# Kernel tuning notes

Measured on AMD Instinct MI355X. Metric: run time of the kernel, lower is better.

## Reference

```python
import jax, jax.numpy as jnp
import numpy as np

N_NODES = 100000
N_EDGES = 1000000
D_IN = 64
D_OUT = 64


def setup_inputs() -> dict:
    key = jax.random.key(0)
    k1, k2, k3, k4, k5 = jax.random.split(key, 5)
    x = jax.random.normal(k1, (N_NODES, D_IN), dtype=jnp.float32)
    W = jax.random.normal(k2, (D_OUT, D_IN), dtype=jnp.float32) / np.sqrt(D_IN)
    edge_weights = jax.random.uniform(k3, (N_EDGES,), dtype=jnp.float32)
    source = jax.random.randint(k4, (N_EDGES,), 0, N_NODES, dtype=jnp.int64 if jax.config.read('jax_enable_x64') else jnp.int32)
    target = jax.random.randint(k5, (N_EDGES,), 0, N_NODES, dtype=jnp.int64 if jax.config.read('jax_enable_x64') else jnp.int32)
    return {"x": x, "W": W, "edge_weights": edge_weights,
            "source": source, "target": target, "num_nodes": N_NODES}


def reference(x, W, edge_weights, source, target, num_nodes):
    # Linear (no bias): h = x @ W^T, shape (num_nodes, out)
    h = jnp.einsum('nd,od->no', x, W)
    # Gather messages per edge, scale by edge weights
    msg = h[source] * edge_weights[:, None]  # (num_edges, out)
    # Scatter-add by target node (sum aggregation)
    delta = jax.ops.segment_sum(msg, target, num_segments=num_nodes)
    return delta
```

## Files before the change

### kernel.cpp

```cpp
#include <hip/hip_runtime.h>


#define D     64
#define BKT   128
#define NBMAX 1024
#define CAP   2048

__global__ __launch_bounds__(256) void gcn_scatter_kernel(
    const float* __restrict__ x, const float* __restrict__ ew,
    const int* __restrict__ src, const int* __restrict__ tgt,
    float* __restrict__ s, int n_edges)
{
    int lane = threadIdx.x & 63;
    int e = blockIdx.x * 4 + (threadIdx.x >> 6);
    if (e >= n_edges) return;
    int sn = src[e];
    int tn = tgt[e];
    float w = ew[e];
    float v = x[(size_t)sn * D + lane] * w;
    atomicAdd(&s[(size_t)tn * D + lane], v);
}

__global__ __launch_bounds__(256) void gcn_gemm_kernel(
    const float* __restrict__ s, const float* __restrict__ W,
    float* __restrict__ out, int n_nodes)
{
    __shared__ float4 xs[64 * 17];
    const int tid  = threadIdx.x;
    const int lane = tid & 63;
    const int wid  = __builtin_amdgcn_readfirstlane(tid >> 6);
    const int row0 = blockIdx.x * 64;

    const float4* s4 = reinterpret_cast<const float4*>(s);
#pragma unroll
    for (int k = 0; k < 4; ++k) {
        int f  = tid + k * 256;
        int r  = f >> 4;
        int c4 = f & 15;
        float4 v = make_float4(0.f, 0.f, 0.f, 0.f);
        if (row0 + r < n_nodes)
            v = s4[(size_t)(row0 + r) * 16 + c4];
        xs[r * 17 + c4] = v;
    }
    __syncthreads();

    float acc[16];
#pragma unroll
    for (int j = 0; j < 16; ++j) acc[j] = 0.f;

    const int o0 = wid * 16;
    const float4* W4 = reinterpret_cast<const float4*>(W);
#pragma unroll
    for (int d4 = 0; d4 < 16; ++d4) {
        float4 xv = xs[lane * 17 + d4];
#pragma unroll
        for (int j = 0; j < 16; ++j) {
            float4 wv = W4[(size_t)(o0 + j) * 16 + d4];
            acc[j] += xv.x * wv.x + xv.y * wv.y + xv.z * wv.z + xv.w * wv.w;
        }
    }

    const int row = row0 + lane;
    if (row < n_nodes) {
        float4* out4 = reinterpret_cast<float4*>(out);
#pragma unroll
        for (int j4 = 0; j4 < 4; ++j4) {
            float4 v = make_float4(acc[j4 * 4 + 0], acc[j4 * 4 + 1],
                                   acc[j4 * 4 + 2], acc[j4 * 4 + 3]);
            out4[(size_t)row * 16 + wid * 4 + j4] = v;
        }
    }
}

__global__ __launch_bounds__(256) void bucket_hist_kernel(
    const int* __restrict__ tgt, int* __restrict__ bcnt,
    int n_edges, int nb, int epb)
{
    __shared__ int h[NBMAX];
    const int tid = threadIdx.x;
    for (int i = tid; i < nb; i += 256) h[i] = 0;
    __syncthreads();
    const int e0 = blockIdx.x * epb;
    const int e1 = min(e0 + epb, n_edges);
    for (int e = e0 + tid; e < e1; e += 256)
        atomicAdd(&h[tgt[e] >> 7], 1);
    __syncthreads();
    for (int b = tid; b < nb; b += 256) {
        int c = h[b];
        if (c) atomicAdd(&bcnt[b], c);
    }
}

__global__ __launch_bounds__(1024) void bucket_scan_kernel(
    const int* __restrict__ bcnt, int* __restrict__ bstarts,
    int* __restrict__ bcur, int nb)
{
    __shared__ int lds[1024];
    const int tid = threadIdx.x;
    int v = (tid < nb) ? bcnt[tid] : 0;
    lds[tid] = v;
    __syncthreads();
    for (int off = 1; off < 1024; off <<= 1) {
        int a = (tid >= off) ? lds[tid - off] : 0;
        __syncthreads();
        lds[tid] += a;
        __syncthreads();
    }
    if (tid < nb) {
        int st = lds[tid] - v;
        bstarts[tid] = st;
        bcur[tid]    = st;
    }
}

__global__ __launch_bounds__(256) void bucket_scatter_kernel(
    const int* __restrict__ src, const int* __restrict__ tgt,
    const float* __restrict__ ew, int* __restrict__ bcur,
    int2* __restrict__ pairs, int n_edges, int nb, int epb)
{
    __shared__ int h[NBMAX];
    __shared__ int base[NBMAX];
    const int tid = threadIdx.x;
    for (int i = tid; i < nb; i += 256) h[i] = 0;
    __syncthreads();
    const int e0 = blockIdx.x * epb;
    const int e1 = min(e0 + epb, n_edges);

    for (int e = e0 + tid; e < e1; e += 256)
        atomicAdd(&h[tgt[e] >> 7], 1);
    __syncthreads();

    for (int b = tid; b < nb; b += 256) {
        int c = h[b];
        base[b] = c ? atomicAdd(&bcur[b], c) : 0;
        h[b] = 0;
    }
    __syncthreads();

    for (int e = e0 + tid; e < e1; e += 256) {
        int t = tgt[e];
        int b = t >> 7;
        int r = atomicAdd(&h[b], 1);
        pairs[base[b] + r] =
            make_int2(((t & (BKT - 1)) << 24) | src[e], __float_as_int(ew[e]));
    }
}

__global__ __launch_bounds__(512, 8) void bucket_sort_reduce_gemm_kernel(
    const float* __restrict__ x, const float* __restrict__ W,
    const int* __restrict__ bstarts, const int2* __restrict__ pairs,
    float* __restrict__ out, int n_nodes, int n_edges, int nb)
{
    __shared__ float Wl[64 * 66];
    __shared__ int2  ep[CAP];
    __shared__ int   segIncl[BKT];
    __shared__ int   rankc[BKT];
    __shared__ float accRow[8][64];

    const int tid  = threadIdx.x;
    const int lane = tid & 63;
    const int wv   = tid >> 6;

    for (int i = tid; i < 64 * 64; i += 512)
        Wl[(i >> 6) * 66 + (i & 63)] = W[i];

    const int b   = blockIdx.x;
    const int beg = bstarts[b];
    const int end = (b + 1 < nb) ? bstarts[b + 1] : n_edges;

    float acc[16];
#pragma unroll
    for (int s = 0; s < 16; ++s) acc[s] = 0.f;

    for (int cbeg = beg; cbeg < end; cbeg += CAP) {
        const int ccnt = min(CAP, end - cbeg);

        if (tid < BKT) segIncl[tid] = 0;
        __syncthreads();

        for (int i = tid; i < ccnt; i += 512) {
            unsigned px = (unsigned)pairs[cbeg + i].x;
            atomicAdd(&segIncl[px >> 24], 1);
        }
        __syncthreads();

        int myc = (tid < BKT) ? segIncl[tid] : 0;
        __syncthreads();
        for (int off = 1; off < BKT; off <<= 1) {
            int a = (tid < BKT && tid >= off) ? segIncl[tid - off] : 0;
            __syncthreads();
            if (tid < BKT) segIncl[tid] += a;
            __syncthreads();
        }
        if (tid < BKT) rankc[tid] = segIncl[tid] - myc;
        __syncthreads();

        for (int i = tid; i < ccnt; i += 512) {
            int2 p = pairs[cbeg + i];
            int tl = ((unsigned)p.x) >> 24;
            int pos = atomicAdd(&rankc[tl], 1);
            ep[pos] = p;
        }
        __syncthreads();

#pragma unroll
        for (int s = 0; s < 16; ++s) {
            const int tl = s * 8 + wv;
            const int s0 = __builtin_amdgcn_readfirstlane(tl ? segIncl[tl - 1] : 0);
            const int s1 = __builtin_amdgcn_readfirstlane(segIncl[tl]);
            float a = acc[s];
            int e = s0;
            for (; e + 4 <= s1; e += 4) {
                int2 q0 = ep[e + 0]; int2 q1 = ep[e + 1];
                int2 q2 = ep[e + 2]; int2 q3 = ep[e + 3];
                int   i0 = __builtin_amdgcn_readfirstlane(q0.x) & 0xFFFFFF;
                int   i1 = __builtin_amdgcn_readfirstlane(q1.x) & 0xFFFFFF;
                int   i2 = __builtin_amdgcn_readfirstlane(q2.x) & 0xFFFFFF;
                int   i3 = __builtin_amdgcn_readfirstlane(q3.x) & 0xFFFFFF;
                float w0 = __int_as_float(__builtin_amdgcn_readfirstlane(q0.y));
                float w1 = __int_as_float(__builtin_amdgcn_readfirstlane(q1.y));
                float w2 = __int_as_float(__builtin_amdgcn_readfirstlane(q2.y));
                float w3 = __int_as_float(__builtin_amdgcn_readfirstlane(q3.y));
                float x0 = x[(size_t)i0 * D + lane];
                float x1 = x[(size_t)i1 * D + lane];
                float x2 = x[(size_t)i2 * D + lane];
                float x3 = x[(size_t)i3 * D + lane];
                a += w0 * x0; a += w1 * x1; a += w2 * x2; a += w3 * x3;
            }
            for (; e < s1; ++e) {
                int2 q = ep[e];
                int   i0 = __builtin_amdgcn_readfirstlane(q.x) & 0xFFFFFF;
                float w0 = __int_as_float(__builtin_amdgcn_readfirstlane(q.y));
                a += w0 * x[(size_t)i0 * D + lane];
            }
            acc[s] = a;
        }
        __syncthreads();
    }

    const int node0 = b * BKT;
#pragma unroll
    for (int s = 0; s < 16; ++s) {
        const int tl = s * 8 + wv;
        const int node = node0 + tl;
        if (node < n_nodes) {
            accRow[wv][lane] = acc[s];
            asm volatile("s_waitcnt lgkmcnt(0)" ::: "memory");
            float o = 0.f;
            const float2* a2 = reinterpret_cast<const float2*>(&accRow[wv][0]);
            const float2* w2 = reinterpret_cast<const float2*>(&Wl[lane * 66]);
#pragma unroll
            for (int d2 = 0; d2 < 32; ++d2) {
                float2 aq = a2[d2];
                float2 wq = w2[d2];
                o += aq.x * wq.x + aq.y * wq.y;
            }
            out[(size_t)node * D + lane] = o;
            asm volatile("s_waitcnt lgkmcnt(0)" ::: "memory");
        }
    }
}

extern "C" void kernel_launch(void* const* d_in, const int* in_sizes, int n_in,
                              void* d_out, int out_size, void* d_ws, size_t ws_size,
                              hipStream_t stream)
{
    const float* x   = (const float*)d_in[0];
    const float* W   = (const float*)d_in[1];
    const float* ew  = (const float*)d_in[2];
    const int*   src = (const int*)d_in[3];
    const int*   tgt = (const int*)d_in[4];

    const int n_nodes = in_sizes[0] / D;
    const int n_edges = in_sizes[2];
    const int nb = (n_nodes + BKT - 1) / BKT;

    int*  bcnt    = (int*)d_ws;
    int*  bstarts = bcnt + NBMAX;
    int*  bcur    = bstarts + NBMAX;
    int2* pairs   = (int2*)(bcur + NBMAX);

    const size_t need = (size_t)3 * NBMAX * sizeof(int) +
                        (size_t)n_edges * sizeof(int2);

    if (nb > NBMAX || n_nodes > (1 << 24) || ws_size < need) {
        float* s = (float*)d_ws;
        hipMemsetAsync(s, 0, (size_t)n_nodes * D * sizeof(float), stream);
        gcn_scatter_kernel<<<(n_edges + 3) / 4, 256, 0, stream>>>(x, ew, src, tgt, s, n_edges);
        gcn_gemm_kernel<<<(n_nodes + 63) / 64, 256, 0, stream>>>(s, W, (float*)d_out, n_nodes);
        return;
    }

    hipMemsetAsync(bcnt, 0, (size_t)nb * sizeof(int), stream);

    const int ablocks = 128;
    const int epbA = (n_edges + ablocks - 1) / ablocks;
    bucket_hist_kernel<<<ablocks, 256, 0, stream>>>(tgt, bcnt, n_edges, nb, epbA);

    bucket_scan_kernel<<<1, 1024, 0, stream>>>(bcnt, bstarts, bcur, nb);

    const int cblocks = 256;
    const int epbC = (n_edges + cblocks - 1) / cblocks;
    bucket_scatter_kernel<<<cblocks, 256, 0, stream>>>(src, tgt, ew, bcur,
                                                       pairs, n_edges, nb, epbC);

    bucket_sort_reduce_gemm_kernel<<<nb, 512, 0, stream>>>(
        x, W, bstarts, pairs, (float*)d_out, n_nodes, n_edges, nb);
}
```

Baseline: 129.5 us.

## Halve bucket size and gather four edges per wave with float4 loads

Buckets shrink from 128 to 64 target nodes, giving about 1563 buckets and therefore more blocks in the fused sort-reduce-GEMM kernel. The bucket scan now handles two entries per thread so it covers up to 2048 buckets. The gather loop now splits each wave into four 16-lane groups, each loading a full 64-float row as float4 for a different edge. Partial sums are combined with cross-lane shuffles before the per-node GEMV, which trades scalar per-edge readfirstlane loads for wider vector loads plus a shuffle reduction. The scatter grid size and occupancy bound are also adjusted.

```diff
diff --git a/kernel.cpp b/kernel.cpp
--- a/kernel.cpp
+++ b/kernel.cpp
@@ -2,9 +2,10 @@
 
 
 #define D     64
-#define BKT   128
-#define NBMAX 1024
-#define CAP   2048
+#define BKT   64
+#define BSH   6
+#define NBMAX 2048
+#define CAP   1024
 
 __global__ __launch_bounds__(256) void gcn_scatter_kernel(
     const float* __restrict__ x, const float* __restrict__ ew,
@@ -83,7 +84,7 @@
     const int e0 = blockIdx.x * epb;
     const int e1 = min(e0 + epb, n_edges);
     for (int e = e0 + tid; e < e1; e += 256)
-        atomicAdd(&h[tgt[e] >> 7], 1);
+        atomicAdd(&h[tgt[e] >> BSH], 1);
     __syncthreads();
     for (int b = tid; b < nb; b += 256) {
         int c = h[b];
@@ -97,8 +98,11 @@
 {
     __shared__ int lds[1024];
     const int tid = threadIdx.x;
-    int v = (tid < nb) ? bcnt[tid] : 0;
-    lds[tid] = v;
+    const int i0 = 2 * tid, i1 = 2 * tid + 1;
+    int v0 = (i0 < nb) ? bcnt[i0] : 0;
+    int v1 = (i1 < nb) ? bcnt[i1] : 0;
+    int tsum = v0 + v1;
+    lds[tid] = tsum;
     __syncthreads();
     for (int off = 1; off < 1024; off <<= 1) {
         int a = (tid >= off) ? lds[tid - off] : 0;
@@ -106,11 +110,9 @@
         lds[tid] += a;
         __syncthreads();
     }
-    if (tid < nb) {
-        int st = lds[tid] - v;
-        bstarts[tid] = st;
-        bcur[tid]    = st;
-    }
+    int pre = lds[tid] - tsum;
+    if (i0 < nb) { bstarts[i0] = pre;      bcur[i0] = pre; }
+    if (i1 < nb) { bstarts[i1] = pre + v0; bcur[i1] = pre + v0; }
 }
 
 __global__ __launch_bounds__(256) void bucket_scatter_kernel(
@@ -127,7 +129,7 @@
     const int e1 = min(e0 + epb, n_edges);
 
     for (int e = e0 + tid; e < e1; e += 256)
-        atomicAdd(&h[tgt[e] >> 7], 1);
+        atomicAdd(&h[tgt[e] >> BSH], 1);
     __syncthreads();
 
     for (int b = tid; b < nb; b += 256) {
@@ -139,14 +141,14 @@
 
     for (int e = e0 + tid; e < e1; e += 256) {
         int t = tgt[e];
-        int b = t >> 7;
+        int b = t >> BSH;
         int r = atomicAdd(&h[b], 1);
         pairs[base[b] + r] =
             make_int2(((t & (BKT - 1)) << 24) | src[e], __float_as_int(ew[e]));
     }
 }
 
-__global__ __launch_bounds__(512, 8) void bucket_sort_reduce_gemm_kernel(
+__global__ __launch_bounds__(512, 6) void bucket_sort_reduce_gemm_kernel(
     const float* __restrict__ x, const float* __restrict__ W,
     const int* __restrict__ bstarts, const int2* __restrict__ pairs,
     float* __restrict__ out, int n_nodes, int n_edges, int nb)
@@ -160,6 +162,8 @@
     const int tid  = threadIdx.x;
     const int lane = tid & 63;
     const int wv   = tid >> 6;
+    const int q4   = lane >> 4;
+    const int m    = lane & 15;
 
     for (int i = tid; i < 64 * 64; i += 512)
         Wl[(i >> 6) * 66 + (i & 63)] = W[i];
@@ -168,9 +172,11 @@
     const int beg = bstarts[b];
     const int end = (b + 1 < nb) ? bstarts[b + 1] : n_edges;
 
-    float acc[16];
-#pragma unroll
-    for (int s = 0; s < 16; ++s) acc[s] = 0.f;
+    float4 acc[8];
+#pragma unroll
+    for (int s = 0; s < 8; ++s) acc[s] = make_float4(0.f, 0.f, 0.f, 0.f);
+
+    const float4* x4 = reinterpret_cast<const float4*>(x);
 
     for (int cbeg = beg; cbeg < end; cbeg += CAP) {
         const int ccnt = min(CAP, end - cbeg);
@@ -204,34 +210,24 @@
         __syncthreads();
 
 #pragma unroll
-        for (int s = 0; s < 16; ++s) {
+        for (int s = 0; s < 8; ++s) {
             const int tl = s * 8 + wv;
             const int s0 = __builtin_amdgcn_readfirstlane(tl ? segIncl[tl - 1] : 0);
             const int s1 = __builtin_amdgcn_readfirstlane(segIncl[tl]);
-            float a = acc[s];
-            int e = s0;
-            for (; e + 4 <= s1; e += 4) {
-                int2 q0 = ep[e + 0]; int2 q1 = ep[e + 1];
-                int2 q2 = ep[e + 2]; int2 q3 = ep[e + 3];
-                int   i0 = __builtin_amdgcn_readfirstlane(q0.x) & 0xFFFFFF;
-                int   i1 = __builtin_amdgcn_readfirstlane(q1.x) & 0xFFFFFF;
-                int   i2 = __builtin_amdgcn_readfirstlane(q2.x) & 0xFFFFFF;
-                int   i3 = __builtin_amdgcn_readfirstlane(q3.x) & 0xFFFFFF;
-                float w0 = __int_as_float(__builtin_amdgcn_readfirstlane(q0.y));
-                float w1 = __int_as_float(__builtin_amdgcn_readfirstlane(q1.y));
-                float w2 = __int_as_float(__builtin_amdgcn_readfirstlane(q2.y));
-                float w3 = __int_as_float(__builtin_amdgcn_readfirstlane(q3.y));
-                float x0 = x[(size_t)i0 * D + lane];
-                float x1 = x[(size_t)i1 * D + lane];
-                float x2 = x[(size_t)i2 * D + lane];
-                float x3 = x[(size_t)i3 * D + lane];
-                a += w0 * x0; a += w1 * x1; a += w2 * x2; a += w3 * x3;
-            }
-            for (; e < s1; ++e) {
-                int2 q = ep[e];
-                int   i0 = __builtin_amdgcn_readfirstlane(q.x) & 0xFFFFFF;
-                float w0 = __int_as_float(__builtin_amdgcn_readfirstlane(q.y));
-                a += w0 * x[(size_t)i0 * D + lane];
+            float4 a = acc[s];
+            for (int e = s0; e < s1; e += 8) {
+                const int ea = e + q4;
+                const int eb = e + 4 + q4;
+                int2 p0 = ep[min(ea, s1 - 1)];
+                int2 p1 = ep[min(eb, s1 - 1)];
+                float w0 = (ea < s1) ? __int_as_float(p0.y) : 0.f;
+                float w1 = (eb < s1) ? __int_as_float(p1.y) : 0.f;
+                float4 xv0 = x4[(size_t)(p0.x & 0xFFFFFF) * 16 + m];
+                float4 xv1 = x4[(size_t)(p1.x & 0xFFFFFF) * 16 + m];
+                a.x += w0 * xv0.x; a.y += w0 * xv0.y;
+                a.z += w0 * xv0.z; a.w += w0 * xv0.w;
+                a.x += w1 * xv1.x; a.y += w1 * xv1.y;
+                a.z += w1 * xv1.z; a.w += w1 * xv1.w;
             }
             acc[s] = a;
         }
@@ -240,12 +236,18 @@
 
     const int node0 = b * BKT;
 #pragma unroll
-    for (int s = 0; s < 16; ++s) {
-        const int tl = s * 8 + wv;
-        const int node = node0 + tl;
+    for (int s = 0; s < 8; ++s) {
+        const int node = node0 + s * 8 + wv;
         if (node < n_nodes) {
-            accRow[wv][lane] = acc[s];
+            float4 a = acc[s];
+            a.x += __shfl_xor(a.x, 16); a.y += __shfl_xor(a.y, 16);
+            a.z += __shfl_xor(a.z, 16); a.w += __shfl_xor(a.w, 16);
+            a.x += __shfl_xor(a.x, 32); a.y += __shfl_xor(a.y, 32);
+            a.z += __shfl_xor(a.z, 32); a.w += __shfl_xor(a.w, 32);
+            if (lane < 16)
+                *reinterpret_cast<float4*>(&accRow[wv][m * 4]) = a;
             asm volatile("s_waitcnt lgkmcnt(0)" ::: "memory");
+
             float o = 0.f;
             const float2* a2 = reinterpret_cast<const float2*>(&accRow[wv][0]);
             const float2* w2 = reinterpret_cast<const float2*>(&Wl[lane * 66]);
@@ -299,7 +301,7 @@
 
     bucket_scan_kernel<<<1, 1024, 0, stream>>>(bcnt, bstarts, bcur, nb);
 
-    const int cblocks = 256;
+    const int cblocks = 128;
     const int epbC = (n_edges + cblocks - 1) / cblocks;
     bucket_scatter_kernel<<<cblocks, 256, 0, stream>>>(src, tgt, ew, bcur,
                                                        pairs, n_edges, nb, epbC);
```

Measured after the change: 139.5 us. 1.08x slower.
